# Kernel tuning notes

Hardware: AMD Instinct MI355X
Metric: run time of the kernel (lower is better)

Reference implementation:

```python
import jax, jax.numpy as jnp
import numpy as np

B, N, F_IN, F_OUT, H = 8, 1024, 64, 128, 4
D = F_OUT // H  # head_dim = 32
NEG_SLOPE = 0.2


def setup_inputs() -> dict:
    key = jax.random.key(0)
    k1, k2, k3, k4, k5 = jax.random.split(key, 5)
    x = jax.random.normal(k1, (B, N, F_IN), dtype=jnp.float32)
    adj = jax.random.randint(k2, (N, N), 0, 2, dtype=jnp.int32)
    edge_weights = jax.random.uniform(k3, (N, N), dtype=jnp.float32)
    W = jax.random.normal(k4, (F_IN, F_OUT), dtype=jnp.float32) * (1.0 / np.sqrt(F_IN))
    a = jax.random.normal(k5, (H, 2 * D), dtype=jnp.float32) * (1.0 / np.sqrt(2 * D))
    return {"x": x, "adj": adj, "edge_weights": edge_weights, "W": W, "a": a}


def reference(x, adj, edge_weights, W, a):
    # x: [B,N,F_in], adj: [N,N] int, edge_weights: [N,N], W: [F_in,F_out], a: [H,2D]
    b, n, _ = x.shape
    h = (x @ W).reshape(b, n, H, D)  # [B,N,H,D]
    # e[b,i,j,h] = leaky_relu(a_src . h_i + a_dst . h_j)  (equivalent to concat trick)
    e_src = jnp.einsum('bnhd,hd->bnh', h, a[:, :D])  # [B,N,H]
    e_dst = jnp.einsum('bnhd,hd->bnh', h, a[:, D:])  # [B,N,H]
    e = jax.nn.leaky_relu(e_src[:, :, None, :] + e_dst[:, None, :, :], NEG_SLOPE)  # [B,N,N,H]
    mask = (adj == 0)[None, :, :, None]  # [1,N,N,1]
    e = jnp.where(mask, -jnp.inf, e)
    # numerically-stable softmax over neighbors (axis=2), matching torch reference
    e_max = jnp.max(e, axis=2, keepdims=True)
    e_max = jnp.where(jnp.isinf(e_max), 0.0, e_max)
    e_stable = e - e_max
    e_stable = jnp.where(jnp.isinf(e_stable), -100.0, e_stable)
    attn = jax.nn.softmax(e_stable, axis=2)
    attn = jnp.where(jnp.isnan(attn), 0.0, attn)
    # dropout is identity in eval mode
    attn = attn * edge_weights[None, :, :, None]  # [B,N,N,H]
    out = jnp.einsum('bijh,bjhd->bihd', attn, h).reshape(b, n, H * D)  # [B,N,F_out]
    avg_attn = attn.mean(axis=-1)  # [B,N,N]
    return out, avg_attn
```

## Files before the change

kernel.cpp:

```cpp
#include <hip/hip_runtime.h>
#include <hip/hip_fp16.h>

constexpr int B  = 8;
constexpr int N  = 1024;
constexpr int FI = 64;
constexpr int FO = 128;
constexpr int NH = 4;
constexpr float LOG2E = 1.4426950408889634f;

using half8 = __attribute__((ext_vector_type(8))) _Float16;
using f32x4 = __attribute__((ext_vector_type(4))) float;

union I8 { int4 v[2]; int s[8]; };
union F8 { float4 v[2]; float s[8]; };

__device__ __forceinline__ unsigned h2pack(float a, float b) {
  __half2 r = __float22half2_rn(make_float2(a, b));
  union { __half2 h; unsigned u; } c; c.h = r; return c.u;
}
__device__ __forceinline__ float h2f(unsigned short u) {
  union { unsigned short s; _Float16 h; } c; c.s = u; return (float)c.h;
}

__global__ __launch_bounds__(256, 2) void gat_prep(
    const float* __restrict__ x, const float* __restrict__ W,
    const float* __restrict__ a, const int* __restrict__ adj,
    const float* __restrict__ ew,
    unsigned short* __restrict__ h16,
    float* __restrict__ es, float* __restrict__ edt,
    unsigned short* __restrict__ mew) {
  const int t = threadIdx.x;
  if (blockIdx.x >= 512) {
    const size_t base = ((size_t)(blockIdx.x - 512) * 256 + t) * 8;
    I8 aj; aj.v[0] = *(const int4*)(adj + base); aj.v[1] = *(const int4*)(adj + base + 4);
    F8 e;  e.v[0]  = *(const float4*)(ew + base); e.v[1]  = *(const float4*)(ew + base + 4);
    union { unsigned short u[8]; uint4 v; } o;
    #pragma unroll
    for (int u = 0; u < 8; ++u) {
      __half hv = __float2half(e.s[u]);
      unsigned short bits = *reinterpret_cast<unsigned short*>(&hv);
      o.u[u] = aj.s[u] ? bits : (unsigned short)0x8000;
    }
    *(uint4*)(mew + base) = o.v;
    return;
  }
  __shared__ float xs[16 * FI];
  const int row0 = blockIdx.x * 16;
  for (int i = t; i < 16 * FI; i += 256) xs[i] = x[row0 * FI + i];
  const int f  = t & 127;
  const int rh = t >> 7;
  float wc[FI];
  #pragma unroll
  for (int k = 0; k < FI; ++k) wc[k] = W[k * FO + f];
  const int hh = f >> 5, d = f & 31;
  const float a_s = a[hh * 64 + d] * LOG2E;
  const float a_d = a[hh * 64 + 32 + d] * LOG2E;
  __syncthreads();
  float acc8[8];
  #pragma unroll
  for (int r = 0; r < 8; ++r) {
    const int lr = rh * 8 + r;
    const float4* xr = (const float4*)(xs + lr * FI);
    float acc = 0.f;
    #pragma unroll
    for (int kq = 0; kq < FI / 4; ++kq) {
      const float4 xv = xr[kq];
      acc += xv.x * wc[4*kq] + xv.y * wc[4*kq+1] + xv.z * wc[4*kq+2] + xv.w * wc[4*kq+3];
    }
    acc8[r] = acc;
    float ps = acc * a_s, pd = acc * a_d;
    #pragma unroll
    for (int off = 16; off; off >>= 1) {
      ps += __shfl_xor(ps, off, 64);
      pd += __shfl_xor(pd, off, 64);
    }
    const int row = row0 + lr;
    if (d == 0) {
      es[row * NH + hh] = ps;
      edt[((size_t)((row >> 10) * NH + hh)) * N + (row & 1023)] = pd;
    }
  }
  const int bb = row0 >> 10;
  const int jl = (row0 & 1023) + rh * 8;
  union { unsigned short u16[8]; uint4 v; } hv;
  #pragma unroll
  for (int r = 0; r < 8; ++r) {
    __half hb = __float2half(acc8[r]);
    hv.u16[r] = *reinterpret_cast<unsigned short*>(&hb);
  }
  const int ft = f >> 4, n = f & 15;
  const int sS = jl >> 5, kq2 = (jl >> 3) & 3;
  const size_t base = (size_t)bb * (FO * N)
                    + ((size_t)(ft * 32 + sS) * 64 + (n + 16 * kq2)) * 8;
  *(uint4*)(h16 + base) = hv.v;
}

__global__ __launch_bounds__(512, 4) void gat_attn(
    const unsigned short* __restrict__ h16,
    const float* __restrict__ es, const float* __restrict__ edt,
    const unsigned short* __restrict__ mew,
    float* __restrict__ out, float* __restrict__ avg) {
  __shared__ unsigned short pew[2][4 * 2048];
  __shared__ float dvl[64];
  const int t  = threadIdx.x;
  const int b  = blockIdx.x & 7;
  const int i0 = (blockIdx.x >> 3) << 4;
  const int il = t >> 5, jq = t & 31;
  const int gi = i0 + il;
  float esv[4];
  { const float4 e4 = *(const float4*)(es + ((size_t)b * N + gi) * NH);
    esv[0] = e4.x; esv[1] = e4.y; esv[2] = e4.z; esv[3] = e4.w; }
  const int lane = t & 63, wave = t >> 6;
  const int hh = wave & 3, nt2 = wave >> 2;
  const int m = lane & 15, kq = lane >> 4;
  const int ft = hh * 2 + nt2;
  const unsigned short* hbp = h16 + (size_t)b * (FO * N) + (size_t)(ft * 32) * 512 + lane * 8;
  f32x4 acc0 = {0.f,0.f,0.f,0.f}, acc1 = {0.f,0.f,0.f,0.f};
  float dpart[4] = {0.f, 0.f, 0.f, 0.f};

  uint2  rmw;
  float4 red[4];
  half8  Bf[4];

  auto ld_p1 = [&](int c) {
    const int jb = c * 128 + jq * 4;
    rmw = *(const uint2*)(mew + (size_t)gi * N + jb);
    #pragma unroll
    for (int h = 0; h < 4; ++h)
      red[h] = *(const float4*)(edt + ((size_t)(b * NH + h)) * N + jb);
  };
  auto ld_B = [&](int c) {
    const size_t so = (size_t)c * 4 * 512;
    #pragma unroll
    for (int ks = 0; ks < 4; ++ks)
      Bf[ks] = *reinterpret_cast<const half8*>(hbp + so + (size_t)ks * 512);
  };
  auto p1_compute = [&](int c) {
    const int buf = c & 1;
    union { uint2 v; unsigned short u[4]; } mw; mw.v = rmw;
    const int g = jq >> 1, half = jq & 1;
    const int o = ((g * 16 + il) ^ (g & 7)) * 8 + half * 4;
    #pragma unroll
    for (int up = 0; up < 2; ++up) {
      float pk[4][2];
      #pragma unroll
      for (int uu = 0; uu < 2; ++uu) {
        const int u = up * 2 + uu;
        const float mfa = h2f((unsigned short)(mw.u[u] & 0x7fff));
        const float sgn = (mw.u[u] >> 15) ? 0.f : 1.f;
        #pragma unroll
        for (int h = 0; h < 4; ++h) {
          float e = esv[h] + (&red[h].x)[u];
          e = fmaxf(e, 0.2f * e);
          const float p = __builtin_amdgcn_exp2f(e);
          pk[h][uu] = p * mfa;
          dpart[h] = fmaf(p, sgn, dpart[h]);
        }
      }
      #pragma unroll
      for (int h = 0; h < 4; ++h)
        *(unsigned*)(pew[buf] + h * 2048 + o + up * 2) = h2pack(pk[h][0], pk[h][1]);
    }
  };
  auto p2_step = [&](int c) {
    const int buf = c & 1;
    #pragma unroll
    for (int ks = 0; ks < 4; ++ks) {
      const int g2 = ks * 4 + kq;
      const int o2 = ((g2 * 16 + m) ^ (g2 & 7)) * 8;
      half8 afr;
      { uint4 tmp = *(const uint4*)(pew[buf] + hh * 2048 + o2);
        __builtin_memcpy(&afr, &tmp, 16); }
      if (ks & 1)
        acc1 = __builtin_amdgcn_mfma_f32_16x16x32_f16(afr, Bf[ks], acc1, 0, 0, 0);
      else
        acc0 = __builtin_amdgcn_mfma_f32_16x16x32_f16(afr, Bf[ks], acc0, 0, 0, 0);
    }
  };

  ld_B(0);
  ld_p1(0);
  p1_compute(0);
  ld_p1(1);
  __syncthreads();

  #pragma unroll 1
  for (int c = 0; c < 8; ++c) {
    p2_step(c);
    if (c + 1 < 8) {
      ld_B(c + 1);
      p1_compute(c + 1);
      if (c + 2 < 8) ld_p1(c + 2);
      __syncthreads();
    }
  }

  #pragma unroll
  for (int h = 0; h < 4; ++h) {
    float v = dpart[h];
    v += __shfl_xor(v, 1, 64);  v += __shfl_xor(v, 2, 64);
    v += __shfl_xor(v, 4, 64);  v += __shfl_xor(v, 8, 64);
    v += __shfl_xor(v, 16, 64);
    if (jq == 0) dvl[il * NH + h] = v;
  }
  __syncthreads();
  if (t < 64) { const float dd = dvl[t]; dvl[t] = dd > 0.f ? 1.0f / dd : 0.f; }
  __syncthreads();
  #pragma unroll
  for (int reg = 0; reg < 4; ++reg) {
    const int row = kq * 4 + reg;
    const float inv = dvl[row * NH + hh];
    out[((size_t)b * N + i0 + row) * FO + hh * 32 + nt2 * 16 + m]
        = (acc0[reg] + acc1[reg]) * inv;
  }
  float inv4[4];
  #pragma unroll
  for (int h = 0; h < 4; ++h) inv4[h] = dvl[il * NH + h];
  #pragma unroll 1
  for (int c = 0; c < 8; ++c) {
    const int jb = c * 128 + jq * 4;
    union { uint2 v; unsigned short u[4]; } mw;
    mw.v = *(const uint2*)(mew + (size_t)gi * N + jb);
    float4 ed4[4];
    #pragma unroll
    for (int h = 0; h < 4; ++h)
      ed4[h] = *(const float4*)(edt + ((size_t)(b * NH + h)) * N + jb);
    float4 r;
    float* rp = &r.x;
    #pragma unroll
    for (int u = 0; u < 4; ++u) {
      const float mfa = h2f((unsigned short)(mw.u[u] & 0x7fff));
      float sv = 0.f;
      #pragma unroll
      for (int h = 0; h < 4; ++h) {
        float e = esv[h] + (&ed4[h].x)[u];
        e = fmaxf(e, 0.2f * e);
        sv += __builtin_amdgcn_exp2f(e) * inv4[h];
      }
      rp[u] = 0.25f * mfa * sv;
    }
    *(float4*)(avg + ((size_t)b * N + gi) * N + jb) = r;
  }
}

extern "C" void kernel_launch(void* const* d_in, const int* in_sizes, int n_in,
                              void* d_out, int out_size, void* d_ws, size_t ws_size,
                              hipStream_t stream) {
  const float* x   = (const float*)d_in[0];
  const int*   adj = (const int*)d_in[1];
  const float* ewt = (const float*)d_in[2];
  const float* W   = (const float*)d_in[3];
  const float* a   = (const float*)d_in[4];

  float* out = (float*)d_out;
  float* avg = out + (size_t)B * N * FO;

  unsigned short* h16 = (unsigned short*)d_ws;
  unsigned short* mew = h16 + (size_t)B * FO * N;
  float* es   = (float*)(mew + (size_t)N * N);
  float* edt  = es + (size_t)B * N * NH;

  gat_prep<<<1024, 256, 0, stream>>>(x, W, a, adj, ewt, h16, es, edt, mew);
  gat_attn<<<B * (N / 16), 512, 0, stream>>>(h16, es, edt, mew, out, avg);
}
```

Baseline: 104.3 us.

## Factor exp2 of leaky-relu scores into per-node exponential products

Computes exp2 of the source and destination scores, and of 0.2 times each, once per node in the prep kernel. The attention kernel then forms p as a product of two precomputed factors, picking the positive or negative branch by testing whether the product reaches 1, so no per-edge exp2 is needed. This removes the per-edge transcendental work. In exchange it adds extra per-node loads, one table in fp16, and a risk of overflow or underflow for large scores.

```diff
diff --git a/kernel.cpp b/kernel.cpp
--- a/kernel.cpp
+++ b/kernel.cpp
@@ -21,13 +21,18 @@
 __device__ __forceinline__ float h2f(unsigned short u) {
   union { unsigned short s; _Float16 h; } c; c.s = u; return (float)c.h;
 }
+__device__ __forceinline__ unsigned short f2h(float f) {
+  __half hv = __float2half(f);
+  return *reinterpret_cast<unsigned short*>(&hv);
+}
 
 __global__ __launch_bounds__(256, 2) void gat_prep(
     const float* __restrict__ x, const float* __restrict__ W,
     const float* __restrict__ a, const int* __restrict__ adj,
     const float* __restrict__ ew,
     unsigned short* __restrict__ h16,
-    float* __restrict__ es, float* __restrict__ edt,
+    float* __restrict__ es1, float* __restrict__ es2,
+    float* __restrict__ ed1, unsigned short* __restrict__ ed2,
     unsigned short* __restrict__ mew) {
   const int t = threadIdx.x;
   if (blockIdx.x >= 512) {
@@ -36,11 +41,8 @@
     F8 e;  e.v[0]  = *(const float4*)(ew + base); e.v[1]  = *(const float4*)(ew + base + 4);
     union { unsigned short u[8]; uint4 v; } o;
     #pragma unroll
-    for (int u = 0; u < 8; ++u) {
-      __half hv = __float2half(e.s[u]);
-      unsigned short bits = *reinterpret_cast<unsigned short*>(&hv);
-      o.u[u] = aj.s[u] ? bits : (unsigned short)0x8000;
-    }
+    for (int u = 0; u < 8; ++u)
+      o.u[u] = aj.s[u] ? f2h(e.s[u]) : (unsigned short)0x8000;
     *(uint4*)(mew + base) = o.v;
     return;
   }
@@ -76,18 +78,18 @@
     }
     const int row = row0 + lr;
     if (d == 0) {
-      es[row * NH + hh] = ps;
-      edt[((size_t)((row >> 10) * NH + hh)) * N + (row & 1023)] = pd;
+      es1[row * NH + hh] = __builtin_amdgcn_exp2f(ps);
+      es2[row * NH + hh] = __builtin_amdgcn_exp2f(0.2f * ps);
+      const size_t eo = ((size_t)((row >> 10) * NH + hh)) * N + (row & 1023);
+      ed1[eo] = __builtin_amdgcn_exp2f(pd);
+      ed2[eo] = f2h(__builtin_amdgcn_exp2f(0.2f * pd));
     }
   }
   const int bb = row0 >> 10;
   const int jl = (row0 & 1023) + rh * 8;
   union { unsigned short u16[8]; uint4 v; } hv;
   #pragma unroll
-  for (int r = 0; r < 8; ++r) {
-    __half hb = __float2half(acc8[r]);
-    hv.u16[r] = *reinterpret_cast<unsigned short*>(&hb);
-  }
+  for (int r = 0; r < 8; ++r) hv.u16[r] = f2h(acc8[r]);
   const int ft = f >> 4, n = f & 15;
   const int sS = jl >> 5, kq2 = (jl >> 3) & 3;
   const size_t base = (size_t)bb * (FO * N)
@@ -97,7 +99,8 @@
 
 __global__ __launch_bounds__(512, 4) void gat_attn(
     const unsigned short* __restrict__ h16,
-    const float* __restrict__ es, const float* __restrict__ edt,
+    const float* __restrict__ es1, const float* __restrict__ es2,
+    const float* __restrict__ ed1, const unsigned short* __restrict__ ed2,
     const unsigned short* __restrict__ mew,
     float* __restrict__ out, float* __restrict__ avg) {
   __shared__ unsigned short pew[2][4 * 2048];
@@ -107,9 +110,11 @@
   const int i0 = (blockIdx.x >> 3) << 4;
   const int il = t >> 5, jq = t & 31;
   const int gi = i0 + il;
-  float esv[4];
-  { const float4 e4 = *(const float4*)(es + ((size_t)b * N + gi) * NH);
-    esv[0] = e4.x; esv[1] = e4.y; esv[2] = e4.z; esv[3] = e4.w; }
+  float g1v[4], g2v[4];
+  { const float4 e4 = *(const float4*)(es1 + ((size_t)b * N + gi) * NH);
+    g1v[0] = e4.x; g1v[1] = e4.y; g1v[2] = e4.z; g1v[3] = e4.w; }
+  { const float4 e4 = *(const float4*)(es2 + ((size_t)b * N + gi) * NH);
+    g2v[0] = e4.x; g2v[1] = e4.y; g2v[2] = e4.z; g2v[3] = e4.w; }
   const int lane = t & 63, wave = t >> 6;
   const int hh = wave & 3, nt2 = wave >> 2;
   const int m = lane & 15, kq = lane >> 4;
@@ -119,15 +124,18 @@
   float dpart[4] = {0.f, 0.f, 0.f, 0.f};
 
   uint2  rmw;
-  float4 red[4];
+  float4 e1r[4];
+  uint2  e2p[4];
   half8  Bf[4];
 
   auto ld_p1 = [&](int c) {
     const int jb = c * 128 + jq * 4;
     rmw = *(const uint2*)(mew + (size_t)gi * N + jb);
     #pragma unroll
-    for (int h = 0; h < 4; ++h)
-      red[h] = *(const float4*)(edt + ((size_t)(b * NH + h)) * N + jb);
+    for (int h = 0; h < 4; ++h) {
+      e1r[h] = *(const float4*)(ed1 + ((size_t)(b * NH + h)) * N + jb);
+      e2p[h] = *(const uint2*)(ed2 + ((size_t)(b * NH + h)) * N + jb);
+    }
   };
   auto ld_B = [&](int c) {
     const size_t so = (size_t)c * 4 * 512;
@@ -150,9 +158,10 @@
         const float sgn = (mw.u[u] >> 15) ? 0.f : 1.f;
         #pragma unroll
         for (int h = 0; h < 4; ++h) {
-          float e = esv[h] + (&red[h].x)[u];
-          e = fmaxf(e, 0.2f * e);
-          const float p = __builtin_amdgcn_exp2f(e);
+          const unsigned w = (u < 2) ? e2p[h].x : e2p[h].y;
+          const float t1 = (&e1r[h].x)[u] * g1v[h];
+          const float t2 = h2f((unsigned short)((u & 1) ? (w >> 16) : (w & 0xffff))) * g2v[h];
+          const float p  = (t1 >= 1.0f) ? t1 : t2;
           pk[h][uu] = p * mfa;
           dpart[h] = fmaf(p, sgn, dpart[h]);
         }
@@ -221,10 +230,12 @@
     const int jb = c * 128 + jq * 4;
     union { uint2 v; unsigned short u[4]; } mw;
     mw.v = *(const uint2*)(mew + (size_t)gi * N + jb);
-    float4 ed4[4];
-    #pragma unroll
-    for (int h = 0; h < 4; ++h)
-      ed4[h] = *(const float4*)(edt + ((size_t)(b * NH + h)) * N + jb);
+    float4 t1r[4]; uint2 t2r[4];
+    #pragma unroll
+    for (int h = 0; h < 4; ++h) {
+      t1r[h] = *(const float4*)(ed1 + ((size_t)(b * NH + h)) * N + jb);
+      t2r[h] = *(const uint2*)(ed2 + ((size_t)(b * NH + h)) * N + jb);
+    }
     float4 r;
     float* rp = &r.x;
     #pragma unroll
@@ -233,9 +244,11 @@
       float sv = 0.f;
       #pragma unroll
       for (int h = 0; h < 4; ++h) {
-        float e = esv[h] + (&ed4[h].x)[u];
-        e = fmaxf(e, 0.2f * e);
-        sv += __builtin_amdgcn_exp2f(e) * inv4[h];
+        const unsigned w = (u < 2) ? t2r[h].x : t2r[h].y;
+        const float t1 = (&t1r[h].x)[u] * g1v[h];
+        const float t2 = h2f((unsigned short)((u & 1) ? (w >> 16) : (w & 0xffff))) * g2v[h];
+        const float p  = (t1 >= 1.0f) ? t1 : t2;
+        sv = fmaf(p, inv4[h], sv);
       }
       rp[u] = 0.25f * mfa * sv;
     }
@@ -257,9 +270,11 @@
 
   unsigned short* h16 = (unsigned short*)d_ws;
   unsigned short* mew = h16 + (size_t)B * FO * N;
-  float* es   = (float*)(mew + (size_t)N * N);
-  float* edt  = es + (size_t)B * N * NH;
-
-  gat_prep<<<1024, 256, 0, stream>>>(x, W, a, adj, ewt, h16, es, edt, mew);
-  gat_attn<<<B * (N / 16), 512, 0, stream>>>(h16, es, edt, mew, out, avg);
-}
+  float* es1 = (float*)(mew + (size_t)N * N);
+  float* es2 = es1 + (size_t)B * N * NH;
+  float* ed1 = es2 + (size_t)B * N * NH;
+  unsigned short* ed2 = (unsigned short*)(ed1 + (size_t)B * NH * N);
+
+  gat_prep<<<1024, 256, 0, stream>>>(x, W, a, adj, ewt, h16, es1, es2, ed1, ed2, mew);
+  gat_attn<<<B * (N / 16), 512, 0, stream>>>(h16, es1, es2, ed1, ed2, mew, out, avg);
+}
```

Measured after the change: 111.6 us. +7.0%, slower.
